# Performance work log

Hardware: AMD Instinct MI355X
Metric: run time of the kernel (lower is better)

## Reference

```python
import jax, jax.numpy as jnp
import numpy as np

B, C, Q, D = 64, 1024, 256, 128
NEG = -1e30  # VERY_NEGATIVE_NUMBER


def setup_inputs() -> dict:
    key = jax.random.key(0)
    k1, k2, k3, k4, k5, k6 = jax.random.split(key, 6)
    return {
        "x_cont": jax.random.normal(k1, (B, C, D), dtype=jnp.float32),
        "x_ques": jax.random.normal(k2, (B, Q, D), dtype=jnp.float32),
        "c_mask": jnp.ones((B, C), dtype=jnp.float32),
        "q_mask": jnp.ones((B, Q), dtype=jnp.float32),
        "W0": jax.random.uniform(k3, (D, 1), jnp.float32, -0.1, 0.1),
        "W1": jax.random.uniform(k4, (D, 1), jnp.float32, -0.1, 0.1),
        "W2": jax.random.uniform(k5, (1, 1, D), jnp.float32, -0.1, 0.1),
        "bias": jnp.zeros((1,), dtype=jnp.float32),
    }


def reference(x_cont, x_ques, c_mask, q_mask, W0, W1, W2, bias):
    # Trilinear similarity S[b,c,q] = x_cont.W0 + x_ques.W1 + (x_cont*W2).x_ques^T + bias
    s0 = x_cont @ W0                                   # [B,C,1]
    s1 = jnp.swapaxes(x_ques @ W1, 1, 2)               # [B,1,Q]
    s2 = jnp.einsum('bcd,bqd->bcq', x_cont * W2, x_ques)  # [B,C,Q]
    S = s0 + s1 + s2 + bias                            # [B,C,Q]

    qm = q_mask[:, None, :]                            # [B,1,Q]
    cm = c_mask[:, :, None]                            # [B,C,1]
    S_ = jax.nn.softmax(S + NEG * (1.0 - qm), axis=-1)           # row softmax [B,C,Q]
    S_T = jnp.swapaxes(jax.nn.softmax(S + NEG * (1.0 - cm), axis=1), 1, 2)  # [B,Q,C]

    c2q = S_ @ x_ques                                  # [B,C,D]
    q2c = (S_ @ S_T) @ x_cont                          # [B,C,D]
    return jnp.concatenate([x_cont, c2q, x_cont * c2q, x_cont * q2c], axis=-1)
```

## Files before the change

kernel.cpp:

```cpp
#include <hip/hip_runtime.h>
#include <math.h>

#define BB 64
#define CC 1024
#define QQ 256
#define DD 128
#define NEGV (-1.0e30f)

typedef short bf8 __attribute__((ext_vector_type(8)));
typedef short bf4 __attribute__((ext_vector_type(4)));
typedef short bf2 __attribute__((ext_vector_type(2)));
typedef float f4v __attribute__((ext_vector_type(4)));

__device__ __forceinline__ short f2bf(float f) {
    unsigned u = __builtin_bit_cast(unsigned, f);
    u += 0x7FFFu + ((u >> 16) & 1u);
    return (short)(u >> 16);
}
__device__ __forceinline__ float bf2f(short s) {
    unsigned u = ((unsigned)(unsigned short)s) << 16;
    return __builtin_bit_cast(float, u);
}

__global__ __launch_bounds__(256) void k0_pre(const float* __restrict__ xc,
                                              const float* __restrict__ xq,
                                              const float* __restrict__ W0,
                                              const float* __restrict__ W1,
                                              const float* __restrict__ W2,
                                              float* __restrict__ s0,
                                              float* __restrict__ s1,
                                              short* __restrict__ xc_bf,
                                              short* __restrict__ xqw_bf) {
    int wid = (blockIdx.x * 256 + threadIdx.x) >> 6;
    int l = threadIdx.x & 63;
    if (wid < BB * CC) {
        const float2* r = (const float2*)(xc + (size_t)wid * DD);
        float2 v = r[l];
        float2 w0 = ((const float2*)W0)[l];
        bf2 o; o.x = f2bf(v.x); o.y = f2bf(v.y);
        *(bf2*)&xc_bf[(size_t)wid * DD + 2 * l] = o;
        float acc = v.x * w0.x + v.y * w0.y;
        #pragma unroll
        for (int off = 1; off < 64; off <<= 1) acc += __shfl_xor(acc, off, 64);
        if (l == 0) s0[wid] = acc;
    } else {
        int rq = wid - BB * CC;
        const float2* r = (const float2*)(xq + (size_t)rq * DD);
        float2 v = r[l];
        float2 w1 = ((const float2*)W1)[l];
        float2 w2 = ((const float2*)W2)[l];
        bf2 o; o.x = f2bf(v.x * w2.x); o.y = f2bf(v.y * w2.y);
        *(bf2*)&xqw_bf[(size_t)rq * DD + 2 * l] = o;
        float acc = v.x * w1.x + v.y * w1.y;
        #pragma unroll
        for (int off = 1; off < 64; off <<= 1) acc += __shfl_xor(acc, off, 64);
        if (l == 0) s1[rq] = acc;
    }
}

__global__ __launch_bounds__(256) void k0_transpose(const float* __restrict__ src,
                                                    short* __restrict__ dst,
                                                    int R, int Cn) {
    __shared__ float tile[64][65];
    int tiles_r = R >> 6, tiles_c = Cn >> 6;
    int per_b = tiles_r * tiles_c;
    int b = blockIdx.x / per_b;
    int rem = blockIdx.x - b * per_b;
    int rt = rem / tiles_c;
    int ct = rem - rt * tiles_c;
    int t = threadIdx.x;
    int c4 = t & 15, rr = t >> 4;
    const float* sb = src + (size_t)b * R * Cn;
    #pragma unroll
    for (int p = 0; p < 4; ++p) {
        int ro = rr + p * 16;
        float4 g = *(const float4*)&sb[(size_t)(rt * 64 + ro) * Cn + ct * 64 + c4 * 4];
        tile[ro][c4 * 4 + 0] = g.x; tile[ro][c4 * 4 + 1] = g.y;
        tile[ro][c4 * 4 + 2] = g.z; tile[ro][c4 * 4 + 3] = g.w;
    }
    __syncthreads();
    short* db = dst + (size_t)b * R * Cn;
    #pragma unroll
    for (int p = 0; p < 4; ++p) {
        int oc = rr + p * 16;
        bf4 o;
        #pragma unroll
        for (int i = 0; i < 4; ++i) o[i] = f2bf(tile[c4 * 4 + i][oc]);
        *(bf4*)&db[(size_t)(ct * 64 + oc) * R + rt * 64 + c4 * 4] = o;
    }
}

#define SCP 1032
#define XAP 136
#define XTP 72

__global__ __launch_bounds__(256, 2) void k1_colsm(
        const short* __restrict__ xc_bf, const short* __restrict__ xcT_bf,
        const short* __restrict__ xqw_bf, const float* __restrict__ s0w,
        const float* __restrict__ c_mask, short* __restrict__ AT) {
    __shared__ __align__(16) short sc[16][SCP];
    __shared__ __align__(16) short pool[64 * XAP + 16 * XAP];
    __shared__ float s0t[64];
    __shared__ float invl[16];
    short (*xa)[XAP]  = (short(*)[XAP])pool;
    short (*xqs)[XAP] = (short(*)[XAP])(pool + 64 * XAP);
    short (*xct)[XTP] = (short(*)[XTP])pool;

    int b = blockIdx.x >> 4, qt = blockIdx.x & 15, q0 = qt * 16;
    int t = threadIdx.x, w = t >> 6, l = t & 63;
    int quad = l >> 4, l16 = l & 15;

    {
        int d8 = t & 15, q = t >> 4;
        *(bf8*)&xqs[q][d8 * 8] =
            *(const bf8*)&xqw_bf[(size_t)((b * QQ + q0 + q) * DD) + d8 * 8];
    }

    for (int ct = 0; ct < 16; ++ct) {
        __syncthreads();
        {
            int d8 = t & 15, cr = t >> 4;
            #pragma unroll
            for (int p = 0; p < 4; ++p)
                *(bf8*)&xa[cr + p * 16][d8 * 8] =
                    *(const bf8*)&xc_bf[(size_t)((b * CC + ct * 64 + cr + p * 16) * DD) + d8 * 8];
            if (t < 64)
                s0t[t] = s0w[b * CC + ct * 64 + t] + NEGV * (1.0f - c_mask[b * CC + ct * 64 + t]);
        }
        __syncthreads();
        f4v acc = {0.f, 0.f, 0.f, 0.f};
        #pragma unroll
        for (int ks = 0; ks < 4; ++ks) {
            bf8 a = *(const bf8*)&xa[w * 16 + l16][ks * 32 + quad * 8];
            bf8 bb = *(const bf8*)&xqs[l16][ks * 32 + quad * 8];
            acc = __builtin_amdgcn_mfma_f32_16x16x32_bf16(a, bb, acc, 0, 0, 0);
        }
        bf4 ov;
        #pragma unroll
        for (int r = 0; r < 4; ++r) ov[r] = f2bf(acc[r] + s0t[w * 16 + quad * 4 + r]);
        *(bf4*)&sc[l16][ct * 64 + w * 16 + quad * 4] = ov;
    }
    __syncthreads();

    {
        int q = t >> 4, k = t & 15;
        float m = -3.0e38f;
        #pragma unroll 8
        for (int i = 0; i < 64; ++i) m = fmaxf(m, bf2f(sc[q][k + 16 * i]));
        #pragma unroll
        for (int off = 1; off < 16; off <<= 1) m = fmaxf(m, __shfl_xor(m, off, 64));
        float sum = 0.f;
        #pragma unroll 8
        for (int i = 0; i < 64; ++i) {
            int idx = k + 16 * i;
            float e = __expf(bf2f(sc[q][idx]) - m);
            sc[q][idx] = f2bf(e);
            sum += e;
        }
        #pragma unroll
        for (int off = 1; off < 16; off <<= 1) sum += __shfl_xor(sum, off, 64);
        if (k == 0) invl[q] = 1.0f / sum;
    }

    f4v acc0 = {0.f, 0.f, 0.f, 0.f}, acc1 = {0.f, 0.f, 0.f, 0.f};
    for (int ct = 0; ct < 16; ++ct) {
        __syncthreads();
        {
            int c8 = t & 7, dr = t >> 3;
            #pragma unroll
            for (int p = 0; p < 4; ++p)
                *(bf8*)&xct[dr + p * 32][c8 * 8] =
                    *(const bf8*)&xcT_bf[(size_t)((b * DD + dr + p * 32) * CC) + ct * 64 + c8 * 8];
        }
        __syncthreads();
        #pragma unroll
        for (int ks = 0; ks < 2; ++ks) {
            bf8 a = *(const bf8*)&sc[l16][ct * 64 + ks * 32 + quad * 8];
            bf8 b0 = *(const bf8*)&xct[w * 32 + l16][ks * 32 + quad * 8];
            acc0 = __builtin_amdgcn_mfma_f32_16x16x32_bf16(a, b0, acc0, 0, 0, 0);
            bf8 b1 = *(const bf8*)&xct[w * 32 + 16 + l16][ks * 32 + quad * 8];
            acc1 = __builtin_amdgcn_mfma_f32_16x16x32_bf16(a, b1, acc1, 0, 0, 0);
        }
    }
    {
        bf4 o0, o1;
        #pragma unroll
        for (int r = 0; r < 4; ++r) {
            float il = invl[quad * 4 + r];
            o0[r] = f2bf(acc0[r] * il);
            o1[r] = f2bf(acc1[r] * il);
        }
        int d0 = w * 32 + l16;
        *(bf4*)&AT[(size_t)((b * DD + d0) * QQ) + q0 + quad * 4] = o0;
        *(bf4*)&AT[(size_t)((b * DD + d0 + 16) * QQ) + q0 + quad * 4] = o1;
    }
}

#define S2P 264

__global__ __launch_bounds__(256, 2) void k2_rowsm(
        const float* __restrict__ xc, const short* __restrict__ xc_bf,
        const short* __restrict__ xqw_bf, const short* __restrict__ xqT_bf,
        const short* __restrict__ AT, const float* __restrict__ s1w,
        const float* __restrict__ q_mask, float* __restrict__ out) {
    __shared__ __align__(16) short sc2[32][S2P];
    __shared__ __align__(16) short pool[32 * XAP + 64 * XAP];
    __shared__ float s1t[QQ];
    __shared__ float invl2[32];
    short (*xa2)[XAP] = (short(*)[XAP])pool;
    short (*xqt)[XAP] = (short(*)[XAP])(pool + 32 * XAP);
    short (*tT)[XTP]  = (short(*)[XTP])pool;

    int b = blockIdx.x >> 5, cb = blockIdx.x & 31, c0g = cb * 32;
    int t = threadIdx.x, w = t >> 6, l = t & 63;
    int quad = l >> 4, l16 = l & 15;

    {
        int d8 = t & 15, cr = t >> 4;
        #pragma unroll
        for (int p = 0; p < 2; ++p)
            *(bf8*)&xa2[cr + p * 16][d8 * 8] =
                *(const bf8*)&xc_bf[(size_t)((b * CC + c0g + cr + p * 16) * DD) + d8 * 8];
        s1t[t] = s1w[b * QQ + t] + NEGV * (1.0f - q_mask[b * QQ + t]);
    }

    for (int qt = 0; qt < 4; ++qt) {
        __syncthreads();
        {
            int d8 = t & 15, qr = t >> 4;
            #pragma unroll
            for (int p = 0; p < 4; ++p)
                *(bf8*)&xqt[qr + p * 16][d8 * 8] =
                    *(const bf8*)&xqw_bf[(size_t)((b * QQ + qt * 64 + qr + p * 16) * DD) + d8 * 8];
        }
        __syncthreads();
        f4v acc0 = {0.f, 0.f, 0.f, 0.f}, acc1 = {0.f, 0.f, 0.f, 0.f};
        #pragma unroll
        for (int ks = 0; ks < 4; ++ks) {
            bf8 a = *(const bf8*)&xqt[w * 16 + l16][ks * 32 + quad * 8];
            bf8 b0 = *(const bf8*)&xa2[l16][ks * 32 + quad * 8];
            acc0 = __builtin_amdgcn_mfma_f32_16x16x32_bf16(a, b0, acc0, 0, 0, 0);
            bf8 b1 = *(const bf8*)&xa2[16 + l16][ks * 32 + quad * 8];
            acc1 = __builtin_amdgcn_mfma_f32_16x16x32_bf16(a, b1, acc1, 0, 0, 0);
        }
        int qbase = qt * 64 + w * 16 + quad * 4;
        bf4 o0, o1;
        #pragma unroll
        for (int r = 0; r < 4; ++r) {
            float sv = s1t[qbase + r];
            o0[r] = f2bf(acc0[r] + sv);
            o1[r] = f2bf(acc1[r] + sv);
        }
        *(bf4*)&sc2[l16][qbase] = o0;
        *(bf4*)&sc2[16 + l16][qbase] = o1;
    }
    __syncthreads();

    {
        int c = t >> 3, k = t & 7;
        float m = -3.0e38f;
        #pragma unroll 8
        for (int i = 0; i < 32; ++i) m = fmaxf(m, bf2f(sc2[c][k + 8 * i]));
        #pragma unroll
        for (int off = 1; off < 8; off <<= 1) m = fmaxf(m, __shfl_xor(m, off, 64));
        float sum = 0.f;
        #pragma unroll 8
        for (int i = 0; i < 32; ++i) {
            int idx = k + 8 * i;
            float e = __expf(bf2f(sc2[c][idx]) - m);
            sc2[c][idx] = f2bf(e);
            sum += e;
        }
        #pragma unroll
        for (int off = 1; off < 8; off <<= 1) sum += __shfl_xor(sum, off, 64);
        if (k == 0) invl2[c] = 1.0f / sum;
    }

    int cb16 = (w & 1) * 16, dh = (w >> 1) * 64;
    f4v ac[4], aq[4];
    f4v zz = {0.f, 0.f, 0.f, 0.f};
    #pragma unroll
    for (int n = 0; n < 4; ++n) { ac[n] = zz; aq[n] = zz; }
    for (int qt = 0; qt < 4; ++qt) {
        __syncthreads();
        {
            int q8 = t & 7, dr = t >> 3;
            #pragma unroll
            for (int p = 0; p < 4; ++p)
                *(bf8*)&tT[dr + p * 32][q8 * 8] =
                    *(const bf8*)&xqT_bf[(size_t)((b * DD + dr + p * 32) * QQ) + qt * 64 + q8 * 8];
        }
        __syncthreads();
        #pragma unroll
        for (int ks = 0; ks < 2; ++ks) {
            bf8 a = *(const bf8*)&sc2[cb16 + l16][qt * 64 + ks * 32 + quad * 8];
            #pragma unroll
            for (int n = 0; n < 4; ++n) {
                bf8 bb = *(const bf8*)&tT[dh + n * 16 + l16][ks * 32 + quad * 8];
                ac[n] = __builtin_amdgcn_mfma_f32_16x16x32_bf16(a, bb, ac[n], 0, 0, 0);
            }
        }
    }
    for (int qt = 0; qt < 4; ++qt) {
        __syncthreads();
        {
            int q8 = t & 7, dr = t >> 3;
            #pragma unroll
            for (int p = 0; p < 4; ++p)
                *(bf8*)&tT[dr + p * 32][q8 * 8] =
                    *(const bf8*)&AT[(size_t)((b * DD + dr + p * 32) * QQ) + qt * 64 + q8 * 8];
        }
        __syncthreads();
        #pragma unroll
        for (int ks = 0; ks < 2; ++ks) {
            bf8 a = *(const bf8*)&sc2[cb16 + l16][qt * 64 + ks * 32 + quad * 8];
            #pragma unroll
            for (int n = 0; n < 4; ++n) {
                bf8 bb = *(const bf8*)&tT[dh + n * 16 + l16][ks * 32 + quad * 8];
                aq[n] = __builtin_amdgcn_mfma_f32_16x16x32_bf16(a, bb, aq[n], 0, 0, 0);
            }
        }
    }

    #pragma unroll
    for (int r = 0; r < 4; ++r) {
        int c = c0g + cb16 + quad * 4 + r;
        float il = invl2[cb16 + quad * 4 + r];
        const float* xrow = xc + (size_t)(b * CC + c) * DD;
        float* orow = out + (size_t)(b * CC + c) * (4 * DD);
        #pragma unroll
        for (int n = 0; n < 4; ++n) {
            int d = dh + n * 16 + l16;
            float xv = xrow[d];
            float c2v = ac[n][r] * il;
            float q2v = aq[n][r] * il;
            orow[d] = xv;
            orow[DD + d] = c2v;
            orow[2 * DD + d] = xv * c2v;
            orow[3 * DD + d] = xv * q2v;
        }
    }
}

extern "C" void kernel_launch(void* const* d_in, const int* in_sizes, int n_in,
                              void* d_out, int out_size, void* d_ws, size_t ws_size,
                              hipStream_t stream) {
    const float* x_cont = (const float*)d_in[0];
    const float* x_ques = (const float*)d_in[1];
    const float* c_mask = (const float*)d_in[2];
    const float* q_mask = (const float*)d_in[3];
    const float* W0     = (const float*)d_in[4];
    const float* W1     = (const float*)d_in[5];
    const float* W2     = (const float*)d_in[6];
    float* out = (float*)d_out;

    char* ws = (char*)d_ws;
    float* s0     = (float*)ws;  ws += (size_t)BB * CC * 4;
    float* s1     = (float*)ws;  ws += (size_t)BB * QQ * 4;
    short* xc_bf  = (short*)ws;  ws += (size_t)BB * CC * DD * 2;
    short* xqw_bf = (short*)ws;  ws += (size_t)BB * QQ * DD * 2;
    short* xcT_bf = (short*)ws;  ws += (size_t)BB * CC * DD * 2;
    short* xqT_bf = (short*)ws;  ws += (size_t)BB * QQ * DD * 2;
    short* AT     = (short*)ws;

    k0_pre<<<(BB * CC + BB * QQ) / 4, 256, 0, stream>>>(x_cont, x_ques, W0, W1, W2,
                                                        s0, s1, xc_bf, xqw_bf);
    k0_transpose<<<BB * 16 * 2, 256, 0, stream>>>(x_cont, xcT_bf, CC, DD);
    k0_transpose<<<BB * 4 * 2, 256, 0, stream>>>(x_ques, xqT_bf, QQ, DD);
    k1_colsm<<<BB * 16, 256, 0, stream>>>(xc_bf, xcT_bf, xqw_bf, s0, c_mask, AT);
    k2_rowsm<<<BB * 32, 256, 0, stream>>>(x_cont, xc_bf, xqw_bf, xqT_bf, AT, s1, q_mask, out);
}
```

Baseline: 297.8 us.

## Fuse preprocessing kernels and load MFMA operands directly from global memory

Merges the bf16 conversion, projection dot products, mask folding and transpose into one fused pre-kernel per input, so x_cont and x_ques are each read once instead of twice. In the two main kernels the LDS staging of operand tiles and its per-iteration barriers are removed; operands are loaded straight from global memory into registers, and occupancy hints rise to 4 blocks. Block indices are swizzled to interleave batches across consecutive blocks for cache locality. The trade-off is that cross-wave data reuse now relies on L1/L2 caches instead of shared memory, and extra barriers are added after the softmax phases.

Result: slower. 323.8 us (+8.7%).

```diff
diff --git a/kernel.cpp b/kernel.cpp
--- a/kernel.cpp
+++ b/kernel.cpp
@@ -9,7 +9,6 @@
 
 typedef short bf8 __attribute__((ext_vector_type(8)));
 typedef short bf4 __attribute__((ext_vector_type(4)));
-typedef short bf2 __attribute__((ext_vector_type(2)));
 typedef float f4v __attribute__((ext_vector_type(4)));
 
 __device__ __forceinline__ short f2bf(float f) {
@@ -22,122 +21,94 @@
     return __builtin_bit_cast(float, u);
 }
 
-__global__ __launch_bounds__(256) void k0_pre(const float* __restrict__ xc,
-                                              const float* __restrict__ xq,
-                                              const float* __restrict__ W0,
-                                              const float* __restrict__ W1,
-                                              const float* __restrict__ W2,
-                                              float* __restrict__ s0,
-                                              float* __restrict__ s1,
-                                              short* __restrict__ xc_bf,
-                                              short* __restrict__ xqw_bf) {
-    int wid = (blockIdx.x * 256 + threadIdx.x) >> 6;
-    int l = threadIdx.x & 63;
-    if (wid < BB * CC) {
-        const float2* r = (const float2*)(xc + (size_t)wid * DD);
-        float2 v = r[l];
-        float2 w0 = ((const float2*)W0)[l];
-        bf2 o; o.x = f2bf(v.x); o.y = f2bf(v.y);
-        *(bf2*)&xc_bf[(size_t)wid * DD + 2 * l] = o;
-        float acc = v.x * w0.x + v.y * w0.y;
-        #pragma unroll
-        for (int off = 1; off < 64; off <<= 1) acc += __shfl_xor(acc, off, 64);
-        if (l == 0) s0[wid] = acc;
-    } else {
-        int rq = wid - BB * CC;
-        const float2* r = (const float2*)(xq + (size_t)rq * DD);
-        float2 v = r[l];
-        float2 w1 = ((const float2*)W1)[l];
-        float2 w2 = ((const float2*)W2)[l];
-        bf2 o; o.x = f2bf(v.x * w2.x); o.y = f2bf(v.y * w2.y);
-        *(bf2*)&xqw_bf[(size_t)rq * DD + 2 * l] = o;
-        float acc = v.x * w1.x + v.y * w1.y;
-        #pragma unroll
-        for (int off = 1; off < 64; off <<= 1) acc += __shfl_xor(acc, off, 64);
-        if (l == 0) s1[rq] = acc;
-    }
-}
-
-__global__ __launch_bounds__(256) void k0_transpose(const float* __restrict__ src,
-                                                    short* __restrict__ dst,
-                                                    int R, int Cn) {
-    __shared__ float tile[64][65];
-    int tiles_r = R >> 6, tiles_c = Cn >> 6;
-    int per_b = tiles_r * tiles_c;
-    int b = blockIdx.x / per_b;
-    int rem = blockIdx.x - b * per_b;
-    int rt = rem / tiles_c;
-    int ct = rem - rt * tiles_c;
+template <int MULW2>
+__global__ __launch_bounds__(256, 2) void k0_fused(const float* __restrict__ src,
+                                                   const float* __restrict__ W,
+                                                   const float* __restrict__ W2,
+                                                   const float* __restrict__ mask,
+                                                   float* __restrict__ sm,
+                                                   short* __restrict__ rm,
+                                                   short* __restrict__ tr, int R) {
+    __shared__ float tile[64][132];
+    int tiles = R >> 6;
+    int b = blockIdx.x / tiles, tl = blockIdx.x - b * tiles;
+    int r0 = tl * 64;
     int t = threadIdx.x;
-    int c4 = t & 15, rr = t >> 4;
-    const float* sb = src + (size_t)b * R * Cn;
-    #pragma unroll
-    for (int p = 0; p < 4; ++p) {
-        int ro = rr + p * 16;
-        float4 g = *(const float4*)&sb[(size_t)(rt * 64 + ro) * Cn + ct * 64 + c4 * 4];
-        tile[ro][c4 * 4 + 0] = g.x; tile[ro][c4 * 4 + 1] = g.y;
-        tile[ro][c4 * 4 + 2] = g.z; tile[ro][c4 * 4 + 3] = g.w;
-    }
-    __syncthreads();
-    short* db = dst + (size_t)b * R * Cn;
-    #pragma unroll
-    for (int p = 0; p < 4; ++p) {
-        int oc = rr + p * 16;
+    int c4 = t & 31, rr = t >> 5;
+    float4 wv = ((const float4*)W)[c4];
+    float4 w2v{};
+    if constexpr (MULW2) w2v = ((const float4*)W2)[c4];
+    const float* sb = src + ((size_t)b * R + r0) * DD;
+    #pragma unroll
+    for (int p = 0; p < 8; ++p) {
+        int row = rr + p * 8;
+        float4 g = *(const float4*)&sb[(size_t)row * DD + c4 * 4];
         bf4 o;
-        #pragma unroll
-        for (int i = 0; i < 4; ++i) o[i] = f2bf(tile[c4 * 4 + i][oc]);
-        *(bf4*)&db[(size_t)(ct * 64 + oc) * R + rt * 64 + c4 * 4] = o;
+        if constexpr (MULW2) {
+            o[0] = f2bf(g.x * w2v.x); o[1] = f2bf(g.y * w2v.y);
+            o[2] = f2bf(g.z * w2v.z); o[3] = f2bf(g.w * w2v.w);
+        } else {
+            o[0] = f2bf(g.x); o[1] = f2bf(g.y);
+            o[2] = f2bf(g.z); o[3] = f2bf(g.w);
+        }
+        *(bf4*)&rm[((size_t)(b * R + r0 + row)) * DD + c4 * 4] = o;
+        float part = g.x * wv.x + g.y * wv.y + g.z * wv.z + g.w * wv.w;
+        #pragma unroll
+        for (int off = 1; off < 32; off <<= 1) part += __shfl_xor(part, off, 64);
+        if ((t & 31) == 0)
+            sm[(size_t)b * R + r0 + row] =
+                part + NEGV * (1.0f - mask[(size_t)b * R + r0 + row]);
+        *(float4*)&tile[row][c4 * 4] = g;
+    }
+    __syncthreads();
+    int d = t >> 1, rh = (t & 1) * 32;
+    #pragma unroll
+    for (int k = 0; k < 8; ++k) {
+        bf4 o;
+        #pragma unroll
+        for (int i = 0; i < 4; ++i) o[i] = f2bf(tile[rh + k * 4 + i][d]);
+        *(bf4*)&tr[((size_t)(b * DD + d)) * R + r0 + rh + k * 4] = o;
     }
 }
 
 #define SCP 1032
-#define XAP 136
-#define XTP 72
-
-__global__ __launch_bounds__(256, 2) void k1_colsm(
+#define S2P 264
+
+__global__ __launch_bounds__(256, 4) void k1_colsm(
         const short* __restrict__ xc_bf, const short* __restrict__ xcT_bf,
-        const short* __restrict__ xqw_bf, const float* __restrict__ s0w,
-        const float* __restrict__ c_mask, short* __restrict__ AT) {
+        const short* __restrict__ xqw_bf, const float* __restrict__ s0m,
+        short* __restrict__ AT) {
     __shared__ __align__(16) short sc[16][SCP];
-    __shared__ __align__(16) short pool[64 * XAP + 16 * XAP];
-    __shared__ float s0t[64];
     __shared__ float invl[16];
-    short (*xa)[XAP]  = (short(*)[XAP])pool;
-    short (*xqs)[XAP] = (short(*)[XAP])(pool + 64 * XAP);
-    short (*xct)[XTP] = (short(*)[XTP])pool;
-
-    int b = blockIdx.x >> 4, qt = blockIdx.x & 15, q0 = qt * 16;
+
+    int bid = blockIdx.x;
+    int qt = (bid >> 3) & 15;
+    int b = ((bid >> 7) << 3) | (bid & 7);
+    int q0 = qt * 16;
     int t = threadIdx.x, w = t >> 6, l = t & 63;
     int quad = l >> 4, l16 = l & 15;
 
-    {
-        int d8 = t & 15, q = t >> 4;
-        *(bf8*)&xqs[q][d8 * 8] =
-            *(const bf8*)&xqw_bf[(size_t)((b * QQ + q0 + q) * DD) + d8 * 8];
-    }
-
+    bf8 bq[4];
+    {
+        const short* qp = &xqw_bf[(size_t)(b * QQ + q0 + l16) * DD + quad * 8];
+        #pragma unroll
+        for (int ks = 0; ks < 4; ++ks) bq[ks] = *(const bf8*)&qp[ks * 32];
+    }
+
+    const short* abase = &xc_bf[(size_t)(b * CC + w * 16 + l16) * DD + quad * 8];
+    const float* s0base = &s0m[b * CC + w * 16 + quad * 4];
     for (int ct = 0; ct < 16; ++ct) {
-        __syncthreads();
-        {
-            int d8 = t & 15, cr = t >> 4;
-            #pragma unroll
-            for (int p = 0; p < 4; ++p)
-                *(bf8*)&xa[cr + p * 16][d8 * 8] =
-                    *(const bf8*)&xc_bf[(size_t)((b * CC + ct * 64 + cr + p * 16) * DD) + d8 * 8];
-            if (t < 64)
-                s0t[t] = s0w[b * CC + ct * 64 + t] + NEGV * (1.0f - c_mask[b * CC + ct * 64 + t]);
-        }
-        __syncthreads();
+        const short* ar = abase + (size_t)ct * 64 * DD;
         f4v acc = {0.f, 0.f, 0.f, 0.f};
         #pragma unroll
         for (int ks = 0; ks < 4; ++ks) {
-            bf8 a = *(const bf8*)&xa[w * 16 + l16][ks * 32 + quad * 8];
-            bf8 bb = *(const bf8*)&xqs[l16][ks * 32 + quad * 8];
-            acc = __builtin_amdgcn_mfma_f32_16x16x32_bf16(a, bb, acc, 0, 0, 0);
-        }
+            bf8 a = *(const bf8*)&ar[ks * 32];
+            acc = __builtin_amdgcn_mfma_f32_16x16x32_bf16(a, bq[ks], acc, 0, 0, 0);
+        }
+        f4v s0v = *(const f4v*)&s0base[ct * 64];
         bf4 ov;
         #pragma unroll
-        for (int r = 0; r < 4; ++r) ov[r] = f2bf(acc[r] + s0t[w * 16 + quad * 4 + r]);
+        for (int r = 0; r < 4; ++r) ov[r] = f2bf(acc[r] + s0v[r]);
         *(bf4*)&sc[l16][ct * 64 + w * 16 + quad * 4] = ov;
     }
     __syncthreads();
@@ -161,24 +132,18 @@
         for (int off = 1; off < 16; off <<= 1) sum += __shfl_xor(sum, off, 64);
         if (k == 0) invl[q] = 1.0f / sum;
     }
+    __syncthreads();
 
     f4v acc0 = {0.f, 0.f, 0.f, 0.f}, acc1 = {0.f, 0.f, 0.f, 0.f};
+    const short* b0base = &xcT_bf[(size_t)(b * DD + w * 32 + l16) * CC + quad * 8];
+    const short* b1base = b0base + (size_t)16 * CC;
     for (int ct = 0; ct < 16; ++ct) {
-        __syncthreads();
-        {
-            int c8 = t & 7, dr = t >> 3;
-            #pragma unroll
-            for (int p = 0; p < 4; ++p)
-                *(bf8*)&xct[dr + p * 32][c8 * 8] =
-                    *(const bf8*)&xcT_bf[(size_t)((b * DD + dr + p * 32) * CC) + ct * 64 + c8 * 8];
-        }
-        __syncthreads();
         #pragma unroll
         for (int ks = 0; ks < 2; ++ks) {
             bf8 a = *(const bf8*)&sc[l16][ct * 64 + ks * 32 + quad * 8];
-            bf8 b0 = *(const bf8*)&xct[w * 32 + l16][ks * 32 + quad * 8];
+            bf8 b0 = *(const bf8*)&b0base[ct * 64 + ks * 32];
             acc0 = __builtin_amdgcn_mfma_f32_16x16x32_bf16(a, b0, acc0, 0, 0, 0);
-            bf8 b1 = *(const bf8*)&xct[w * 32 + 16 + l16][ks * 32 + quad * 8];
+            bf8 b1 = *(const bf8*)&b1base[ct * 64 + ks * 32];
             acc1 = __builtin_amdgcn_mfma_f32_16x16x32_bf16(a, b1, acc1, 0, 0, 0);
         }
     }
@@ -191,65 +156,56 @@
             o1[r] = f2bf(acc1[r] * il);
         }
         int d0 = w * 32 + l16;
-        *(bf4*)&AT[(size_t)((b * DD + d0) * QQ) + q0 + quad * 4] = o0;
-        *(bf4*)&AT[(size_t)((b * DD + d0 + 16) * QQ) + q0 + quad * 4] = o1;
-    }
-}
-
-#define S2P 264
-
-__global__ __launch_bounds__(256, 2) void k2_rowsm(
+        *(bf4*)&AT[(size_t)(b * DD + d0) * QQ + q0 + quad * 4] = o0;
+        *(bf4*)&AT[(size_t)(b * DD + d0 + 16) * QQ + q0 + quad * 4] = o1;
+    }
+}
+
+__global__ __launch_bounds__(256, 4) void k2_rowsm(
         const float* __restrict__ xc, const short* __restrict__ xc_bf,
         const short* __restrict__ xqw_bf, const short* __restrict__ xqT_bf,
-        const short* __restrict__ AT, const float* __restrict__ s1w,
-        const float* __restrict__ q_mask, float* __restrict__ out) {
+        const short* __restrict__ AT, const float* __restrict__ s1m,
+        float* __restrict__ out) {
     __shared__ __align__(16) short sc2[32][S2P];
-    __shared__ __align__(16) short pool[32 * XAP + 64 * XAP];
-    __shared__ float s1t[QQ];
     __shared__ float invl2[32];
-    short (*xa2)[XAP] = (short(*)[XAP])pool;
-    short (*xqt)[XAP] = (short(*)[XAP])(pool + 32 * XAP);
-    short (*tT)[XTP]  = (short(*)[XTP])pool;
-
-    int b = blockIdx.x >> 5, cb = blockIdx.x & 31, c0g = cb * 32;
+
+    int bid = blockIdx.x;
+    int cb = (bid >> 3) & 31;
+    int b = ((bid >> 8) << 3) | (bid & 7);
+    int c0g = cb * 32;
     int t = threadIdx.x, w = t >> 6, l = t & 63;
     int quad = l >> 4, l16 = l & 15;
 
-    {
-        int d8 = t & 15, cr = t >> 4;
-        #pragma unroll
-        for (int p = 0; p < 2; ++p)
-            *(bf8*)&xa2[cr + p * 16][d8 * 8] =
-                *(const bf8*)&xc_bf[(size_t)((b * CC + c0g + cr + p * 16) * DD) + d8 * 8];
-        s1t[t] = s1w[b * QQ + t] + NEGV * (1.0f - q_mask[b * QQ + t]);
-    }
-
+    bf8 bc0[4], bc1[4];
+    {
+        const short* p0 = &xc_bf[(size_t)(b * CC + c0g + l16) * DD + quad * 8];
+        const short* p1 = p0 + 16 * DD;
+        #pragma unroll
+        for (int ks = 0; ks < 4; ++ks) {
+            bc0[ks] = *(const bf8*)&p0[ks * 32];
+            bc1[ks] = *(const bf8*)&p1[ks * 32];
+        }
+    }
+
+    const short* abase = &xqw_bf[(size_t)(b * QQ + w * 16 + l16) * DD + quad * 8];
+    const float* s1base = &s1m[b * QQ + w * 16 + quad * 4];
+    #pragma unroll
     for (int qt = 0; qt < 4; ++qt) {
-        __syncthreads();
-        {
-            int d8 = t & 15, qr = t >> 4;
-            #pragma unroll
-            for (int p = 0; p < 4; ++p)
-                *(bf8*)&xqt[qr + p * 16][d8 * 8] =
-                    *(const bf8*)&xqw_bf[(size_t)((b * QQ + qt * 64 + qr + p * 16) * DD) + d8 * 8];
-        }
-        __syncthreads();
+        const short* ar = abase + (size_t)qt * 64 * DD;
         f4v acc0 = {0.f, 0.f, 0.f, 0.f}, acc1 = {0.f, 0.f, 0.f, 0.f};
         #pragma unroll
         for (int ks = 0; ks < 4; ++ks) {
-            bf8 a = *(const bf8*)&xqt[w * 16 + l16][ks * 32 + quad * 8];
-            bf8 b0 = *(const bf8*)&xa2[l16][ks * 32 + quad * 8];
-            acc0 = __builtin_amdgcn_mfma_f32_16x16x32_bf16(a, b0, acc0, 0, 0, 0);
-            bf8 b1 = *(const bf8*)&xa2[16 + l16][ks * 32 + quad * 8];
-            acc1 = __builtin_amdgcn_mfma_f32_16x16x32_bf16(a, b1, acc1, 0, 0, 0);
+            bf8 a = *(const bf8*)&ar[ks * 32];
+            acc0 = __builtin_amdgcn_mfma_f32_16x16x32_bf16(a, bc0[ks], acc0, 0, 0, 0);
+            acc1 = __builtin_amdgcn_mfma_f32_16x16x32_bf16(a, bc1[ks], acc1, 0, 0, 0);
         }
         int qbase = qt * 64 + w * 16 + quad * 4;
+        f4v sv = *(const f4v*)&s1base[qt * 64];
         bf4 o0, o1;
         #pragma unroll
         for (int r = 0; r < 4; ++r) {
-            float sv = s1t[qbase + r];
-            o0[r] = f2bf(acc0[r] + sv);
-            o1[r] = f2bf(acc1[r] + sv);
+            o0[r] = f2bf(acc0[r] + sv[r]);
+            o1[r] = f2bf(acc1[r] + sv[r]);
         }
         *(bf4*)&sc2[l16][qbase] = o0;
         *(bf4*)&sc2[16 + l16][qbase] = o1;
@@ -275,48 +231,28 @@
         for (int off = 1; off < 8; off <<= 1) sum += __shfl_xor(sum, off, 64);
         if (k == 0) invl2[c] = 1.0f / sum;
     }
+    __syncthreads();
 
     int cb16 = (w & 1) * 16, dh = (w >> 1) * 64;
     f4v ac[4], aq[4];
     f4v zz = {0.f, 0.f, 0.f, 0.f};
     #pragma unroll
     for (int n = 0; n < 4; ++n) { ac[n] = zz; aq[n] = zz; }
+    const short* bqt = &xqT_bf[(size_t)(b * DD + dh + l16) * QQ + quad * 8];
+    const short* bat = &AT[(size_t)(b * DD + dh + l16) * QQ + quad * 8];
+    #pragma unroll
     for (int qt = 0; qt < 4; ++qt) {
-        __syncthreads();
-        {
-            int q8 = t & 7, dr = t >> 3;
-            #pragma unroll
-            for (int p = 0; p < 4; ++p)
-                *(bf8*)&tT[dr + p * 32][q8 * 8] =
-                    *(const bf8*)&xqT_bf[(size_t)((b * DD + dr + p * 32) * QQ) + qt * 64 + q8 * 8];
-        }
-        __syncthreads();
         #pragma unroll
         for (int ks = 0; ks < 2; ++ks) {
             bf8 a = *(const bf8*)&sc2[cb16 + l16][qt * 64 + ks * 32 + quad * 8];
             #pragma unroll
             for (int n = 0; n < 4; ++n) {
-                bf8 bb = *(const bf8*)&tT[dh + n * 16 + l16][ks * 32 + quad * 8];
+                bf8 bb = *(const bf8*)&bqt[(size_t)(n * 16) * QQ + qt * 64 + ks * 32];
                 ac[n] = __builtin_amdgcn_mfma_f32_16x16x32_bf16(a, bb, ac[n], 0, 0, 0);
             }
-        }
-    }
-    for (int qt = 0; qt < 4; ++qt) {
-        __syncthreads();
-        {
-            int q8 = t & 7, dr = t >> 3;
-            #pragma unroll
-            for (int p = 0; p < 4; ++p)
-                *(bf8*)&tT[dr + p * 32][q8 * 8] =
-                    *(const bf8*)&AT[(size_t)((b * DD + dr + p * 32) * QQ) + qt * 64 + q8 * 8];
-        }
-        __syncthreads();
-        #pragma unroll
-        for (int ks = 0; ks < 2; ++ks) {
-            bf8 a = *(const bf8*)&sc2[cb16 + l16][qt * 64 + ks * 32 + quad * 8];
             #pragma unroll
             for (int n = 0; n < 4; ++n) {
-                bf8 bb = *(const bf8*)&tT[dh + n * 16 + l16][ks * 32 + quad * 8];
+                bf8 bb = *(const bf8*)&bat[(size_t)(n * 16) * QQ + qt * 64 + ks * 32];
                 aq[n] = __builtin_amdgcn_mfma_f32_16x16x32_bf16(a, bb, aq[n], 0, 0, 0);
             }
         }
@@ -355,18 +291,18 @@
     float* out = (float*)d_out;
 
     char* ws = (char*)d_ws;
-    float* s0     = (float*)ws;  ws += (size_t)BB * CC * 4;
-    float* s1     = (float*)ws;  ws += (size_t)BB * QQ * 4;
+    float* s0m    = (float*)ws;  ws += (size_t)BB * CC * 4;
+    float* s1m    = (float*)ws;  ws += (size_t)BB * QQ * 4;
     short* xc_bf  = (short*)ws;  ws += (size_t)BB * CC * DD * 2;
     short* xqw_bf = (short*)ws;  ws += (size_t)BB * QQ * DD * 2;
     short* xcT_bf = (short*)ws;  ws += (size_t)BB * CC * DD * 2;
     short* xqT_bf = (short*)ws;  ws += (size_t)BB * QQ * DD * 2;
     short* AT     = (short*)ws;
 
-    k0_pre<<<(BB * CC + BB * QQ) / 4, 256, 0, stream>>>(x_cont, x_ques, W0, W1, W2,
-                                                        s0, s1, xc_bf, xqw_bf);
-    k0_transpose<<<BB * 16 * 2, 256, 0, stream>>>(x_cont, xcT_bf, CC, DD);
-    k0_transpose<<<BB * 4 * 2, 256, 0, stream>>>(x_ques, xqT_bf, QQ, DD);
-    k1_colsm<<<BB * 16, 256, 0, stream>>>(xc_bf, xcT_bf, xqw_bf, s0, c_mask, AT);
-    k2_rowsm<<<BB * 32, 256, 0, stream>>>(x_cont, xc_bf, xqw_bf, xqT_bf, AT, s1, q_mask, out);
-}
+    k0_fused<0><<<BB * (CC / 64), 256, 0, stream>>>(x_cont, W0, nullptr, c_mask,
+                                                    s0m, xc_bf, xcT_bf, CC);
+    k0_fused<1><<<BB * (QQ / 64), 256, 0, stream>>>(x_ques, W1, W2, q_mask,
+                                                    s1m, xqw_bf, xqT_bf, QQ);
+    k1_colsm<<<BB * 16, 256, 0, stream>>>(xc_bf, xcT_bf, xqw_bf, s0m, AT);
+    k2_rowsm<<<BB * 32, 256, 0, stream>>>(x_cont, xc_bf, xqw_bf, xqT_bf, AT, s1m, out);
+}
```
